# Performance work log

Measured on AMD Instinct MI355X. Metric: run time of the kernel, lower is better.

## Reference

```python
import jax, jax.numpy as jnp
import numpy as np

B, H, W, C = 16, 64, 64, 512
WS, SS, NH = 8, 4, 16
HD = C // NH
N = WS * WS          # tokens per window = 64
NWH, NWW = H // WS, W // WS
NW = NWH * NWW       # windows per image = 64
HID = 2048
EPS = 1e-5

def _rel_pos_index():
    coords = np.stack(np.meshgrid(np.arange(WS), np.arange(WS), indexing='ij'))  # [2,ws,ws]
    cf = coords.reshape(2, -1)                      # [2,N]
    rel = cf[:, :, None] - cf[:, None, :]           # [2,N,N]
    rel = rel.transpose(1, 2, 0).astype(np.int64)   # [N,N,2]
    rel[:, :, 0] += WS - 1
    rel[:, :, 1] += WS - 1
    rel[:, :, 0] *= 2 * WS - 1
    return rel.sum(-1)                              # [N,N]

def _attn_mask():
    img = np.zeros((H, W), dtype=np.float32)
    cnt = 0
    sls = (slice(0, -WS), slice(-WS, -SS), slice(-SS, None))
    for hs in sls:
        for ws_ in sls:
            img[hs, ws_] = cnt
            cnt += 1
    mw = img.reshape(NWH, WS, NWW, WS).transpose(0, 2, 1, 3).reshape(-1, N)  # [nW,N]
    am = mw[:, None, :] - mw[:, :, None]            # [nW,N,N] (unsqueeze(1)-unsqueeze(2))
    return np.where(am != 0, np.float32(-100.0), np.float32(0.0))

_RPI = jnp.asarray(_rel_pos_index())
_AMASK = jnp.asarray(_attn_mask())

def _ln(x, g, b):
    m = jnp.mean(x, -1, keepdims=True)
    v = jnp.mean((x - m) ** 2, -1, keepdims=True)
    return (x - m) * jax.lax.rsqrt(v + EPS) * g + b

def setup_inputs() -> dict:
    key = jax.random.key(0)
    ks = jax.random.split(key, 8)
    s = 0.02
    return {
        'x': jax.random.normal(ks[0], (B, H * W, C), jnp.float32),
        'g1': jnp.ones((C,), jnp.float32), 'b1': jnp.zeros((C,), jnp.float32),
        'qkv_w': jax.random.normal(ks[1], (C, 3 * C), jnp.float32) * s,
        'qkv_b': jnp.zeros((3 * C,), jnp.float32),
        'proj_w': jax.random.normal(ks[2], (C, C), jnp.float32) * s,
        'proj_b': jnp.zeros((C,), jnp.float32),
        'rpb': jax.random.normal(ks[3], ((2 * WS - 1) ** 2, NH), jnp.float32) * s,
        'g2': jnp.ones((C,), jnp.float32), 'b2': jnp.zeros((C,), jnp.float32),
        'fc1_w': jax.random.normal(ks[4], (C, HID), jnp.float32) * s,
        'fc1_b': jnp.zeros((HID,), jnp.float32),
        'fc2_w': jax.random.normal(ks[5], (HID, C), jnp.float32) * s,
        'fc2_b': jnp.zeros((C,), jnp.float32),
    }

def reference(x, g1, b1, qkv_w, qkv_b, proj_w, proj_b, rpb, g2, b2, fc1_w, fc1_b, fc2_w, fc2_b):
    shortcut = x                                    # [B,L,C]
    xn = _ln(x, g1, b1).reshape(B, H, W, C)
    xs = jnp.roll(xn, (-SS, -SS), axis=(1, 2))      # cyclic shift
    # window partition -> [B*nW, N, C]
    xw = xs.reshape(B, NWH, WS, NWW, WS, C).transpose(0, 1, 3, 2, 4, 5).reshape(-1, N, C)
    # attention
    qkv = xw @ qkv_w + qkv_b                        # [Bw,N,3C]
    qkv = qkv.reshape(-1, N, 3, NH, HD).transpose(2, 0, 3, 1, 4)  # [3,Bw,NH,N,HD]
    q, k, v = qkv[0], qkv[1], qkv[2]
    scale = jnp.asarray(HD ** -0.5, xw.dtype)
    attn = jnp.einsum('bhnd,bhmd->bhnm', q, k) * scale            # [Bw,NH,N,N]
    bias = rpb[_RPI.reshape(-1)].reshape(N, N, NH).transpose(2, 0, 1)
    attn = attn + bias[None]
    attn = attn.reshape(B, NW, NH, N, N) + _AMASK[None, :, None]
    attn = jax.nn.softmax(attn.reshape(-1, NH, N, N), axis=-1)
    out = jnp.einsum('bhnm,bhmd->bhnd', attn, v)    # [Bw,NH,N,HD]
    out = out.transpose(0, 2, 1, 3).reshape(-1, N, C)
    out = out @ proj_w + proj_b
    # window reverse -> [B,H,W,C]
    xr = out.reshape(B, NWH, NWW, WS, WS, C).transpose(0, 1, 3, 2, 4, 5).reshape(B, H, W, C)
    xr = jnp.roll(xr, (SS, SS), axis=(1, 2)).reshape(B, H * W, C)
    x = shortcut + xr
    h = _ln(x, g2, b2)
    h = jax.nn.gelu(h @ fc1_w + fc1_b, approximate=False) @ fc2_w + fc2_b
    return x + h
```

## Files before the change

kernel.cpp:

```cpp
#include <hip/hip_runtime.h>
#include <hip/hip_bf16.h>

using f32x4  = __attribute__((ext_vector_type(4))) float;
using bf16x8 = __attribute__((ext_vector_type(8))) short;
using short8 = __attribute__((ext_vector_type(8))) short;
using s16x4  = __attribute__((ext_vector_type(4))) short;

#define DEVINL __device__ __forceinline__

DEVINL short f2bf(float f) {
  unsigned u = __builtin_bit_cast(unsigned, f);
  u += 0x7fffu + ((u >> 16) & 1u);
  return (short)(u >> 16);
}

DEVINL float gelu_fast(float v) {
  float t = __expf(-1.5957691216057308f * (v + 0.044715f * v * v * v));
  return v * __builtin_amdgcn_rcpf(1.0f + t);
}

#define GLDS16(g, l) __builtin_amdgcn_global_load_lds( \
    (const __attribute__((address_space(1))) void*)(g), \
    (__attribute__((address_space(3))) void*)(l), 16, 0, 0)

__global__ __launch_bounds__(256)
void transpose_bf16(const float* __restrict__ in, short* __restrict__ out, int R, int C) {
  int idx = blockIdx.x * 256 + threadIdx.x;
  if (idx >= R * C) return;
  int c = idx / R, r = idx % R;
  out[idx] = f2bf(in[(size_t)r * C + c]);
}

__global__ __launch_bounds__(256)
void bias_expand(const float* __restrict__ rpb, float* __restrict__ BIASF) {
  int idx = blockIdx.x * 256 + threadIdx.x;
  int head = idx >> 12, n = (idx >> 6) & 63, m = idx & 63;
  int i1 = n >> 3, j1 = n & 7, i2 = m >> 3, j2 = m & 7;
  BIASF[idx] = rpb[((i1 - i2 + 7) * 15 + (j1 - j2 + 7)) * 16 + head];
}

template<int REMAP>
__global__ __launch_bounds__(256)
void ln_kernel(const float* __restrict__ X, const float* __restrict__ gamma,
               const float* __restrict__ beta, short* __restrict__ OUT) {
  const int lane = threadIdx.x & 63;
  const int wid  = threadIdx.x >> 6;
  const int t    = blockIdx.x * 4 + wid;
  const float* xp = X + (size_t)t * 512 + lane * 8;
  float4 a = *(const float4*)xp;
  float4 b = *(const float4*)(xp + 4);
  float s = a.x + a.y + a.z + a.w + b.x + b.y + b.z + b.w;
  float q = a.x*a.x + a.y*a.y + a.z*a.z + a.w*a.w
          + b.x*b.x + b.y*b.y + b.z*b.z + b.w*b.w;
#pragma unroll
  for (int d = 1; d < 64; d <<= 1) { s += __shfl_xor(s, d); q += __shfl_xor(q, d); }
  float mean = s * (1.0f / 512.0f);
  float var  = q * (1.0f / 512.0f) - mean * mean;
  float rstd = rsqrtf(var + 1e-5f);
  float4 g0 = *(const float4*)(gamma + lane * 8);
  float4 g1 = *(const float4*)(gamma + lane * 8 + 4);
  float4 b0 = *(const float4*)(beta + lane * 8);
  float4 b1 = *(const float4*)(beta + lane * 8 + 4);
  short8 o;
  o[0] = f2bf((a.x - mean) * rstd * g0.x + b0.x);
  o[1] = f2bf((a.y - mean) * rstd * g0.y + b0.y);
  o[2] = f2bf((a.z - mean) * rstd * g0.z + b0.z);
  o[3] = f2bf((a.w - mean) * rstd * g0.w + b0.w);
  o[4] = f2bf((b.x - mean) * rstd * g1.x + b1.x);
  o[5] = f2bf((b.y - mean) * rstd * g1.y + b1.y);
  o[6] = f2bf((b.z - mean) * rstd * g1.z + b1.z);
  o[7] = f2bf((b.w - mean) * rstd * g1.w + b1.w);
  size_t orow;
  if (REMAP) {
    int bb = t >> 12, l = t & 4095, hh = l >> 6, ww = l & 63;
    int hs = (hh + 60) & 63, ws2 = (ww + 60) & 63;
    orow = (size_t)(bb * 64 + (hs >> 3) * 8 + (ws2 >> 3)) * 64 + (hs & 7) * 8 + (ws2 & 7);
  } else {
    orow = (size_t)t;
  }
  *(short8*)(OUT + orow * 512 + lane * 8) = o;
}

__global__ __launch_bounds__(256)
void attn_core(const short* __restrict__ Q, const short* __restrict__ Kb,
               const short* __restrict__ VT, const float* __restrict__ BIASF,
               short* __restrict__ AOUT) {
  __shared__ short P[4][4096];
  const int tid = threadIdx.x, lane = tid & 63, wid = tid >> 6;
  const int lr = lane & 15, lg = lane >> 4;
  const int gw = blockIdx.x * 4 + wid;
  const int win = gw >> 4, head = gw & 15;
  const int wimg = win & 63, wh = wimg >> 3, ww = wimg & 7;
  const size_t qbase = (size_t)win * 64 * 512 + head * 32;
  short* Pb = P[wid];

  bf16x8 aq[4], bk[4];
#pragma unroll
  for (int tm = 0; tm < 4; ++tm) aq[tm] = *(const bf16x8*)(Q  + qbase + (size_t)(tm * 16 + lr) * 512 + lg * 8);
#pragma unroll
  for (int tn = 0; tn < 4; ++tn) bk[tn] = *(const bf16x8*)(Kb + qbase + (size_t)(tn * 16 + lr) * 512 + lg * 8);
  f32x4 sa[4][4] = {};
#pragma unroll
  for (int tm = 0; tm < 4; ++tm)
#pragma unroll
    for (int tn = 0; tn < 4; ++tn)
      sa[tm][tn] = __builtin_amdgcn_mfma_f32_16x16x32_bf16(aq[tm], bk[tn], sa[tm][tn], 0, 0, 0);

  const float* bias_h = BIASF + head * 4096;
  float inv[4][4];
#pragma unroll
  for (int tm = 0; tm < 4; ++tm) {
#pragma unroll
    for (int e = 0; e < 4; ++e) {
      const int n = tm * 16 + lg * 4 + e;
      const int i1 = n >> 3, j1 = n & 7;
      const int rh1 = (wh == 7) ? 1 + (i1 >> 2) : 0;
      const int rw1 = (ww == 7) ? 1 + (j1 >> 2) : 0;
      float v[4];
      float mx = -3.0e38f;
#pragma unroll
      for (int tn = 0; tn < 4; ++tn) {
        const int m = tn * 16 + lr;
        const int mi = (m >> 3), mj = m & 7;
        const int rh2 = (wh == 7) ? 1 + (mi >> 2) : 0;
        const int rw2 = (ww == 7) ? 1 + (mj >> 2) : 0;
        float val = sa[tm][tn][e] + bias_h[n * 64 + m]
                  + ((rh1 != rh2 || rw1 != rw2) ? -100.0f : 0.0f);
        v[tn] = val;
        mx = fmaxf(mx, val);
      }
#pragma unroll
      for (int d = 1; d < 16; d <<= 1) mx = fmaxf(mx, __shfl_xor(mx, d));
      float sum = 0.f;
#pragma unroll
      for (int tn = 0; tn < 4; ++tn) { v[tn] = __expf(v[tn] - mx); sum += v[tn]; }
#pragma unroll
      for (int d = 1; d < 16; d <<= 1) sum += __shfl_xor(sum, d);
      inv[tm][e] = 1.0f / sum;
      const int sw = (n & 7) << 3;
#pragma unroll
      for (int tn = 0; tn < 4; ++tn) Pb[n * 64 + ((tn * 16 + lr) ^ sw)] = f2bf(v[tn]);
    }
  }
  __syncthreads();

  f32x4 oa[4][2] = {};
  const short* vt = VT + (size_t)win * 32768 + head * 2048;
#pragma unroll
  for (int ks = 0; ks < 2; ++ks) {
    bf16x8 pa[4], bv[2];
#pragma unroll
    for (int tm = 0; tm < 4; ++tm) {
      const int r = tm * 16 + lr;
      pa[tm] = *(const bf16x8*)(Pb + r * 64 + ((ks * 32 + lg * 8) ^ ((r & 7) << 3)));
    }
#pragma unroll
    for (int t2 = 0; t2 < 2; ++t2) bv[t2] = *(const bf16x8*)(vt + (t2 * 16 + lr) * 64 + ks * 32 + lg * 8);
#pragma unroll
    for (int tm = 0; tm < 4; ++tm)
#pragma unroll
      for (int t2 = 0; t2 < 2; ++t2)
        oa[tm][t2] = __builtin_amdgcn_mfma_f32_16x16x32_bf16(pa[tm], bv[t2], oa[tm][t2], 0, 0, 0);
  }
#pragma unroll
  for (int tm = 0; tm < 4; ++tm)
#pragma unroll
    for (int t2 = 0; t2 < 2; ++t2)
#pragma unroll
      for (int e = 0; e < 4; ++e) {
        const int n = tm * 16 + lg * 4 + e;
        AOUT[((size_t)win * 64 + n) * 512 + head * 32 + t2 * 16 + lr] = f2bf(oa[tm][t2][e] * inv[tm][e]);
      }
}

template<int EPI, int K, int NX>
__global__ __launch_bounds__(512, 1)
void gemmBK64(const short* __restrict__ Aa, const short* __restrict__ Bb,
              const float* __restrict__ bias, const float* __restrict__ resid,
              float* __restrict__ outf, short* __restrict__ outh) {
  constexpr int NT = K / 64;
  __shared__ short L[24576];
  const int tid = threadIdx.x;
  const int lane = tid & 63, wid = tid >> 6;
  const int lr = lane & 15, lg = lane >> 4;
  const int wm = wid >> 1, wn = wid & 1;

  const int nwg = gridDim.x;
  const int id = blockIdx.x;
  const int id2 = (id & 7) * (nwg >> 3) + (id >> 3);
  const int mt    = (EPI == 1) ? (id2 % NX) : (id2 / NX);
  const int ntile = (EPI == 1) ? (id2 / NX) : (id2 % NX);
  const int m0 = mt * 256, n0 = ntile * 128;

  const int rr = tid >> 3;
  const int ss = ((tid & 7) ^ (rr & 7)) * 8;
  const short* pA = Aa + (size_t)(m0 + rr) * K + ss;
  const short* pB = Bb + (size_t)(n0 + rr) * K + ss;
  char* Ld = (char*)L + tid * 16;

  const int xr = lr & 7;
  const char* rA0 = (char*)L + (wm * 64 + lr) * 128 + ((lg ^ xr) << 4);
  const char* rA1 = (char*)L + (wm * 64 + lr) * 128 + (((4 + lg) ^ xr) << 4);
  const char* rB0 = (char*)L + 32768 + (wn * 64 + lr) * 128 + ((lg ^ xr) << 4);
  const char* rB1 = (char*)L + 32768 + (wn * 64 + lr) * 128 + (((4 + lg) ^ xr) << 4);

  f32x4 acc[4][4] = {};
  for (int kt = 0; kt < NT; ++kt) {
    const int ko = kt * 64;
    GLDS16(pA + ko,                    Ld);
    GLDS16(pA + ko + (size_t)64  * K,  Ld + 8192);
    GLDS16(pA + ko + (size_t)128 * K,  Ld + 16384);
    GLDS16(pA + ko + (size_t)192 * K,  Ld + 24576);
    GLDS16(pB + ko,                    Ld + 32768);
    GLDS16(pB + ko + (size_t)64  * K,  Ld + 40960);
    __syncthreads();
    bf16x8 a[4], b[4];
#pragma unroll
    for (int i = 0; i < 4; ++i) a[i] = *(const bf16x8*)(rA0 + i * 2048);
#pragma unroll
    for (int j = 0; j < 4; ++j) b[j] = *(const bf16x8*)(rB0 + j * 2048);
#pragma unroll
    for (int i = 0; i < 4; ++i)
#pragma unroll
      for (int j = 0; j < 4; ++j)
        acc[i][j] = __builtin_amdgcn_mfma_f32_16x16x32_bf16(a[i], b[j], acc[i][j], 0, 0, 0);
#pragma unroll
    for (int i = 0; i < 4; ++i) a[i] = *(const bf16x8*)(rA1 + i * 2048);
#pragma unroll
    for (int j = 0; j < 4; ++j) b[j] = *(const bf16x8*)(rB1 + j * 2048);
#pragma unroll
    for (int i = 0; i < 4; ++i)
#pragma unroll
      for (int j = 0; j < 4; ++j)
        acc[i][j] = __builtin_amdgcn_mfma_f32_16x16x32_bf16(a[i], b[j], acc[i][j], 0, 0, 0);
    __syncthreads();
  }

  if (EPI == 1) {
#pragma unroll
    for (int i = 0; i < 4; ++i) {
      const int h0 = m0 + wm * 64 + i * 16 + lg * 4;
      const float4 bi = *(const float4*)(bias + h0);
#pragma unroll
      for (int j = 0; j < 4; ++j) {
        const int tok = n0 + wn * 64 + j * 16 + lr;
        s16x4 o;
        o[0] = f2bf(gelu_fast(acc[i][j][0] + bi.x));
        o[1] = f2bf(gelu_fast(acc[i][j][1] + bi.y));
        o[2] = f2bf(gelu_fast(acc[i][j][2] + bi.z));
        o[3] = f2bf(gelu_fast(acc[i][j][3] + bi.w));
        *(s16x4*)(outh + (size_t)tok * 2048 + h0) = o;
      }
    }
  } else if (EPI == 0) {
#pragma unroll
    for (int j = 0; j < 4; ++j) {
      const int col = n0 + wn * 64 + j * 16 + lr;
      const float bc = bias[col];
#pragma unroll
      for (int i = 0; i < 4; ++i)
#pragma unroll
        for (int e = 0; e < 4; ++e) {
          const int row = m0 + wm * 64 + i * 16 + lg * 4 + e;
          float v = acc[i][j][e] + bc;
          const int wv = row >> 6, n = row & 63;
          const int bb = wv >> 6, wi = wv & 63;
          const int hs = (wi >> 3) * 8 + (n >> 3), ws2 = (wi & 7) * 8 + (n & 7);
          const int hh = (hs + 4) & 63, wwp = (ws2 + 4) & 63;
          const size_t orow = (size_t)bb * 4096 + hh * 64 + wwp;
          outf[orow * 512 + col] = resid[orow * 512 + col] + v;
        }
    }
  } else if (EPI == 2) {
#pragma unroll
    for (int j = 0; j < 4; ++j) {
      const int col = n0 + wn * 64 + j * 16 + lr;
      const float bc = bias[col];
#pragma unroll
      for (int i = 0; i < 4; ++i)
#pragma unroll
        for (int e = 0; e < 4; ++e) {
          const int row = m0 + wm * 64 + i * 16 + lg * 4 + e;
          outf[(size_t)row * 512 + col] = acc[i][j][e] + bc + resid[(size_t)row * 512 + col];
        }
    }
  } else {
    const int seg = n0 >> 9;
#pragma unroll
    for (int j = 0; j < 4; ++j) {
      const int col = n0 + wn * 64 + j * 16 + lr;
      const float bc = bias[col];
#pragma unroll
      for (int i = 0; i < 4; ++i) {
        const int row0 = m0 + wm * 64 + i * 16 + lg * 4;
        if (seg == 2) {
          const int cc = col - 1024;
          s16x4 o;
#pragma unroll
          for (int e = 0; e < 4; ++e) o[e] = f2bf(acc[i][j][e] + bc);
          *(s16x4*)(outh + 67108864 +
                    (size_t)((row0 >> 6) * 16 + (cc >> 5)) * 2048 + (cc & 31) * 64 + (row0 & 63)) = o;
        } else {
#pragma unroll
          for (int e = 0; e < 4; ++e) {
            const int row = row0 + e;
            float v = acc[i][j][e] + bc;
            if (seg == 0) outh[(size_t)row * 512 + col] = f2bf(v * 0.17677669529663687f);
            else          outh[33554432 + (size_t)row * 512 + (col - 512)] = f2bf(v);
          }
        }
      }
    }
  }
}

extern "C" void kernel_launch(void* const* d_in, const int* in_sizes, int n_in,
                              void* d_out, int out_size, void* d_ws, size_t ws_size,
                              hipStream_t stream) {
  (void)in_sizes; (void)n_in; (void)out_size; (void)ws_size;
  const float* x      = (const float*)d_in[0];
  const float* g1     = (const float*)d_in[1];
  const float* b1     = (const float*)d_in[2];
  const float* qkv_w  = (const float*)d_in[3];
  const float* qkv_b  = (const float*)d_in[4];
  const float* proj_w = (const float*)d_in[5];
  const float* proj_b = (const float*)d_in[6];
  const float* rpb    = (const float*)d_in[7];
  const float* g2     = (const float*)d_in[8];
  const float* b2     = (const float*)d_in[9];
  const float* fc1_w  = (const float*)d_in[10];
  const float* fc1_b  = (const float*)d_in[11];
  const float* fc2_w  = (const float*)d_in[12];
  const float* fc2_b  = (const float*)d_in[13];
  float* out = (float*)d_out;
  char* ws = (char*)d_ws;

  short* WQKVT  = (short*)(ws);
  short* WPROJT = (short*)(ws + 1572864);
  short* WFC1T  = (short*)(ws + 2097152);
  short* WFC2T  = (short*)(ws + 4194304);
  float* X2     = (float*)(ws + 6291456);
  float* BIASF  = (float*)(ws + 6291456);
  short* ATT    = (short*)(ws + 140509184);
  short* XW     = (short*)(ws + 207618048);
  short* QB     = (short*)(ws + 274726912);
  short* H1     = XW;
  short* X2N    = ATT;

  transpose_bf16<<<3072, 256, 0, stream>>>(qkv_w,  WQKVT, 512, 1536);
  transpose_bf16<<<1024, 256, 0, stream>>>(proj_w, WPROJT, 512, 512);
  transpose_bf16<<<4096, 256, 0, stream>>>(fc1_w,  WFC1T, 512, 2048);
  transpose_bf16<<<4096, 256, 0, stream>>>(fc2_w,  WFC2T, 2048, 512);
  bias_expand<<<256, 256, 0, stream>>>(rpb, BIASF);

  ln_kernel<1><<<16384, 256, 0, stream>>>(x, g1, b1, XW);
  gemmBK64<3, 512, 12><<<3072, 512, 0, stream>>>(XW, WQKVT, qkv_b, nullptr, nullptr, QB);
  attn_core<<<4096, 256, 0, stream>>>(QB, QB + 33554432, QB + 67108864, BIASF, ATT);
  gemmBK64<0, 512, 4><<<1024, 512, 0, stream>>>(ATT, WPROJT, proj_b, x, X2, nullptr);
  ln_kernel<0><<<16384, 256, 0, stream>>>(X2, g2, b2, X2N);
  gemmBK64<1, 512, 8><<<4096, 512, 0, stream>>>(WFC1T, X2N, fc1_b, nullptr, nullptr, H1);
  gemmBK64<2, 2048, 4><<<1024, 512, 0, stream>>>(H1, WFC2T, fc2_b, X2, out, nullptr);
}
```

Baseline: 843.1 us.

## Store residual stream in bf16 and transpose QKV GEMM operand order

The proj GEMM now writes the post-attention residual X2 as bf16 instead of fp32. A new bf16-input LayerNorm kernel reads it, and the fc2 epilogue reads the bf16 residual back. Separately, the QKV GEMM swaps A/B so weights are the M dimension, and its epilogue is rewritten with vector bias loads and per-element strided V-transpose stores. This cuts memory traffic for the intermediate residual, at the cost of reduced precision in the residual path and a different store pattern for Q/K/V.

Result: no change. 857.7 us (+1.7%).

```diff
diff --git a/kernel.cpp b/kernel.cpp
--- a/kernel.cpp
+++ b/kernel.cpp
@@ -12,6 +12,9 @@
   unsigned u = __builtin_bit_cast(unsigned, f);
   u += 0x7fffu + ((u >> 16) & 1u);
   return (short)(u >> 16);
+}
+DEVINL float bf2f(short h) {
+  return __builtin_bit_cast(float, (unsigned)((unsigned short)h) << 16);
 }
 
 DEVINL float gelu_fast(float v) {
@@ -82,6 +85,40 @@
 }
 
 __global__ __launch_bounds__(256)
+void ln_bf16(const short* __restrict__ X, const float* __restrict__ gamma,
+             const float* __restrict__ beta, short* __restrict__ OUT) {
+  const int lane = threadIdx.x & 63;
+  const int wid  = threadIdx.x >> 6;
+  const int t    = blockIdx.x * 4 + wid;
+  short8 v = *(const short8*)(X + (size_t)t * 512 + lane * 8);
+  float f[8];
+#pragma unroll
+  for (int k = 0; k < 8; ++k) f[k] = bf2f(v[k]);
+  float s = 0.f, q = 0.f;
+#pragma unroll
+  for (int k = 0; k < 8; ++k) { s += f[k]; q += f[k] * f[k]; }
+#pragma unroll
+  for (int d = 1; d < 64; d <<= 1) { s += __shfl_xor(s, d); q += __shfl_xor(q, d); }
+  float mean = s * (1.0f / 512.0f);
+  float var  = q * (1.0f / 512.0f) - mean * mean;
+  float rstd = rsqrtf(var + 1e-5f);
+  float4 g0 = *(const float4*)(gamma + lane * 8);
+  float4 g1 = *(const float4*)(gamma + lane * 8 + 4);
+  float4 b0 = *(const float4*)(beta + lane * 8);
+  float4 b1 = *(const float4*)(beta + lane * 8 + 4);
+  short8 o;
+  o[0] = f2bf((f[0] - mean) * rstd * g0.x + b0.x);
+  o[1] = f2bf((f[1] - mean) * rstd * g0.y + b0.y);
+  o[2] = f2bf((f[2] - mean) * rstd * g0.z + b0.z);
+  o[3] = f2bf((f[3] - mean) * rstd * g0.w + b0.w);
+  o[4] = f2bf((f[4] - mean) * rstd * g1.x + b1.x);
+  o[5] = f2bf((f[5] - mean) * rstd * g1.y + b1.y);
+  o[6] = f2bf((f[6] - mean) * rstd * g1.z + b1.z);
+  o[7] = f2bf((f[7] - mean) * rstd * g1.w + b1.w);
+  *(short8*)(OUT + (size_t)t * 512 + lane * 8) = o;
+}
+
+__global__ __launch_bounds__(256)
 void attn_core(const short* __restrict__ Q, const short* __restrict__ Kb,
                const short* __restrict__ VT, const float* __restrict__ BIASF,
                short* __restrict__ AOUT) {
@@ -177,6 +214,7 @@
 __global__ __launch_bounds__(512, 1)
 void gemmBK64(const short* __restrict__ Aa, const short* __restrict__ Bb,
               const float* __restrict__ bias, const float* __restrict__ resid,
+              const short* __restrict__ residh,
               float* __restrict__ outf, short* __restrict__ outh) {
   constexpr int NT = K / 64;
   __shared__ short L[24576];
@@ -188,8 +226,9 @@
   const int nwg = gridDim.x;
   const int id = blockIdx.x;
   const int id2 = (id & 7) * (nwg >> 3) + (id >> 3);
-  const int mt    = (EPI == 1) ? (id2 % NX) : (id2 / NX);
-  const int ntile = (EPI == 1) ? (id2 / NX) : (id2 % NX);
+  const bool swapped = (EPI == 1 || EPI == 3);
+  const int mt    = swapped ? (id2 % NX) : (id2 / NX);
+  const int ntile = swapped ? (id2 / NX) : (id2 % NX);
   const int m0 = mt * 256, n0 = ntile * 128;
 
   const int rr = tid >> 3;
@@ -268,7 +307,7 @@
           const int hs = (wi >> 3) * 8 + (n >> 3), ws2 = (wi & 7) * 8 + (n & 7);
           const int hh = (hs + 4) & 63, wwp = (ws2 + 4) & 63;
           const size_t orow = (size_t)bb * 4096 + hh * 64 + wwp;
-          outf[orow * 512 + col] = resid[orow * 512 + col] + v;
+          outh[orow * 512 + col] = f2bf(resid[orow * 512 + col] + v);
         }
     }
   } else if (EPI == 2) {
@@ -281,33 +320,42 @@
 #pragma unroll
         for (int e = 0; e < 4; ++e) {
           const int row = m0 + wm * 64 + i * 16 + lg * 4 + e;
-          outf[(size_t)row * 512 + col] = acc[i][j][e] + bc + resid[(size_t)row * 512 + col];
+          outf[(size_t)row * 512 + col] = acc[i][j][e] + bc + bf2f(residh[(size_t)row * 512 + col]);
         }
     }
   } else {
-    const int seg = n0 >> 9;
-#pragma unroll
-    for (int j = 0; j < 4; ++j) {
-      const int col = n0 + wn * 64 + j * 16 + lr;
-      const float bc = bias[col];
-#pragma unroll
-      for (int i = 0; i < 4; ++i) {
-        const int row0 = m0 + wm * 64 + i * 16 + lg * 4;
-        if (seg == 2) {
-          const int cc = col - 1024;
+    const int seg = m0 >> 9;
+    const float qs = 0.17677669529663687f;
+#pragma unroll
+    for (int i = 0; i < 4; ++i) {
+      const int oc0 = m0 + wm * 64 + i * 16 + lg * 4;
+      const float4 bi = *(const float4*)(bias + oc0);
+#pragma unroll
+      for (int j = 0; j < 4; ++j) {
+        const int tok = n0 + wn * 64 + j * 16 + lr;
+        if (seg == 0) {
           s16x4 o;
-#pragma unroll
-          for (int e = 0; e < 4; ++e) o[e] = f2bf(acc[i][j][e] + bc);
-          *(s16x4*)(outh + 67108864 +
-                    (size_t)((row0 >> 6) * 16 + (cc >> 5)) * 2048 + (cc & 31) * 64 + (row0 & 63)) = o;
+          o[0] = f2bf((acc[i][j][0] + bi.x) * qs);
+          o[1] = f2bf((acc[i][j][1] + bi.y) * qs);
+          o[2] = f2bf((acc[i][j][2] + bi.z) * qs);
+          o[3] = f2bf((acc[i][j][3] + bi.w) * qs);
+          *(s16x4*)(outh + (size_t)tok * 512 + oc0) = o;
+        } else if (seg == 1) {
+          s16x4 o;
+          o[0] = f2bf(acc[i][j][0] + bi.x);
+          o[1] = f2bf(acc[i][j][1] + bi.y);
+          o[2] = f2bf(acc[i][j][2] + bi.z);
+          o[3] = f2bf(acc[i][j][3] + bi.w);
+          *(s16x4*)(outh + 33554432 + (size_t)tok * 512 + (oc0 - 512)) = o;
         } else {
-#pragma unroll
-          for (int e = 0; e < 4; ++e) {
-            const int row = row0 + e;
-            float v = acc[i][j][e] + bc;
-            if (seg == 0) outh[(size_t)row * 512 + col] = f2bf(v * 0.17677669529663687f);
-            else          outh[33554432 + (size_t)row * 512 + (col - 512)] = f2bf(v);
-          }
+          const int cc0 = oc0 - 1024;
+          short* vbase = outh + 67108864 +
+              (size_t)((tok >> 6) * 16 + (cc0 >> 5)) * 2048 + (tok & 63);
+          const int d0 = cc0 & 31;
+          vbase[(d0 + 0) * 64] = f2bf(acc[i][j][0] + bi.x);
+          vbase[(d0 + 1) * 64] = f2bf(acc[i][j][1] + bi.y);
+          vbase[(d0 + 2) * 64] = f2bf(acc[i][j][2] + bi.z);
+          vbase[(d0 + 3) * 64] = f2bf(acc[i][j][3] + bi.w);
         }
       }
     }
@@ -339,7 +387,7 @@
   short* WPROJT = (short*)(ws + 1572864);
   short* WFC1T  = (short*)(ws + 2097152);
   short* WFC2T  = (short*)(ws + 4194304);
-  float* X2     = (float*)(ws + 6291456);
+  short* X2B    = (short*)(ws + 6291456);
   float* BIASF  = (float*)(ws + 6291456);
   short* ATT    = (short*)(ws + 140509184);
   short* XW     = (short*)(ws + 207618048);
@@ -354,10 +402,10 @@
   bias_expand<<<256, 256, 0, stream>>>(rpb, BIASF);
 
   ln_kernel<1><<<16384, 256, 0, stream>>>(x, g1, b1, XW);
-  gemmBK64<3, 512, 12><<<3072, 512, 0, stream>>>(XW, WQKVT, qkv_b, nullptr, nullptr, QB);
+  gemmBK64<3, 512, 6><<<3072, 512, 0, stream>>>(WQKVT, XW, qkv_b, nullptr, nullptr, nullptr, QB);
   attn_core<<<4096, 256, 0, stream>>>(QB, QB + 33554432, QB + 67108864, BIASF, ATT);
-  gemmBK64<0, 512, 4><<<1024, 512, 0, stream>>>(ATT, WPROJT, proj_b, x, X2, nullptr);
-  ln_kernel<0><<<16384, 256, 0, stream>>>(X2, g2, b2, X2N);
-  gemmBK64<1, 512, 8><<<4096, 512, 0, stream>>>(WFC1T, X2N, fc1_b, nullptr, nullptr, H1);
-  gemmBK64<2, 2048, 4><<<1024, 512, 0, stream>>>(H1, WFC2T, fc2_b, X2, out, nullptr);
-}
+  gemmBK64<0, 512, 4><<<1024, 512, 0, stream>>>(ATT, WPROJT, proj_b, x, nullptr, nullptr, X2B);
+  ln_bf16<<<16384, 256, 0, stream>>>(X2B, g2, b2, X2N);
+  gemmBK64<1, 512, 8><<<4096, 512, 0, stream>>>(WFC1T, X2N, fc1_b, nullptr, nullptr, nullptr, H1);
+  gemmBK64<2, 2048, 4><<<1024, 512, 0, stream>>>(H1, WFC2T, fc2_b, nullptr, X2B, out, nullptr);
+}
```

## Swap QKV GEMM operands to emit vectorized Q/K stores; merge prep kernels

Applied to the files above, without the earlier changes.

The QKV projection GEMM now computes the transposed product (weights as the M operand, tokens as the N operand), so each lane's four accumulator values are consecutive output channels. Q and K can then be written as packed 4-element bf16 stores with a vector bias load, replacing the old scalar strided stores. V, whose layout is transposed, goes from one packed store to four scalar stores. The four weight-transpose launches and the bias-expansion launch are folded into a single prep kernel to cut launch overhead.

Result: no change. 846.1 us (+0.3%).

```diff
diff --git a/kernel.cpp b/kernel.cpp
--- a/kernel.cpp
+++ b/kernel.cpp
@@ -24,19 +24,31 @@
     (__attribute__((address_space(3))) void*)(l), 16, 0, 0)
 
 __global__ __launch_bounds__(256)
-void transpose_bf16(const float* __restrict__ in, short* __restrict__ out, int R, int C) {
-  int idx = blockIdx.x * 256 + threadIdx.x;
-  if (idx >= R * C) return;
-  int c = idx / R, r = idx % R;
-  out[idx] = f2bf(in[(size_t)r * C + c]);
-}
-
-__global__ __launch_bounds__(256)
-void bias_expand(const float* __restrict__ rpb, float* __restrict__ BIASF) {
-  int idx = blockIdx.x * 256 + threadIdx.x;
-  int head = idx >> 12, n = (idx >> 6) & 63, m = idx & 63;
-  int i1 = n >> 3, j1 = n & 7, i2 = m >> 3, j2 = m & 7;
-  BIASF[idx] = rpb[((i1 - i2 + 7) * 15 + (j1 - j2 + 7)) * 16 + head];
+void prep(const float* __restrict__ qkv_w, const float* __restrict__ proj_w,
+          const float* __restrict__ fc1_w, const float* __restrict__ fc2_w,
+          const float* __restrict__ rpb,
+          short* __restrict__ WQKVT, short* __restrict__ WPROJT,
+          short* __restrict__ WFC1T, short* __restrict__ WFC2T,
+          float* __restrict__ BIASF) {
+  const int b = blockIdx.x, t = threadIdx.x;
+  if (b < 3072) {
+    int idx = b * 256 + t; int c = idx / 512, r = idx % 512;
+    WQKVT[idx] = f2bf(qkv_w[(size_t)r * 1536 + c]);
+  } else if (b < 4096) {
+    int idx = (b - 3072) * 256 + t; int c = idx / 512, r = idx % 512;
+    WPROJT[idx] = f2bf(proj_w[(size_t)r * 512 + c]);
+  } else if (b < 8192) {
+    int idx = (b - 4096) * 256 + t; int c = idx / 512, r = idx % 512;
+    WFC1T[idx] = f2bf(fc1_w[(size_t)r * 2048 + c]);
+  } else if (b < 12288) {
+    int idx = (b - 8192) * 256 + t; int c = idx / 2048, r = idx % 2048;
+    WFC2T[idx] = f2bf(fc2_w[(size_t)r * 512 + c]);
+  } else {
+    int idx = (b - 12288) * 256 + t;
+    int head = idx >> 12, n = (idx >> 6) & 63, m = idx & 63;
+    int i1 = n >> 3, j1 = n & 7, i2 = m >> 3, j2 = m & 7;
+    BIASF[idx] = rpb[((i1 - i2 + 7) * 15 + (j1 - j2 + 7)) * 16 + head];
+  }
 }
 
 template<int REMAP>
@@ -188,8 +200,9 @@
   const int nwg = gridDim.x;
   const int id = blockIdx.x;
   const int id2 = (id & 7) * (nwg >> 3) + (id >> 3);
-  const int mt    = (EPI == 1) ? (id2 % NX) : (id2 / NX);
-  const int ntile = (EPI == 1) ? (id2 / NX) : (id2 % NX);
+  const bool swapped = (EPI == 1 || EPI == 3);
+  const int mt    = swapped ? (id2 % NX) : (id2 / NX);
+  const int ntile = swapped ? (id2 / NX) : (id2 % NX);
   const int m0 = mt * 256, n0 = ntile * 128;
 
   const int rr = tid >> 3;
@@ -285,29 +298,38 @@
         }
     }
   } else {
-    const int seg = n0 >> 9;
-#pragma unroll
-    for (int j = 0; j < 4; ++j) {
-      const int col = n0 + wn * 64 + j * 16 + lr;
-      const float bc = bias[col];
-#pragma unroll
-      for (int i = 0; i < 4; ++i) {
-        const int row0 = m0 + wm * 64 + i * 16 + lg * 4;
-        if (seg == 2) {
-          const int cc = col - 1024;
+    const int seg = m0 >> 9;
+    const float qs = 0.17677669529663687f;
+#pragma unroll
+    for (int i = 0; i < 4; ++i) {
+      const int oc0 = m0 + wm * 64 + i * 16 + lg * 4;
+      const float4 bi = *(const float4*)(bias + oc0);
+#pragma unroll
+      for (int j = 0; j < 4; ++j) {
+        const int tok = n0 + wn * 64 + j * 16 + lr;
+        if (seg == 0) {
           s16x4 o;
-#pragma unroll
-          for (int e = 0; e < 4; ++e) o[e] = f2bf(acc[i][j][e] + bc);
-          *(s16x4*)(outh + 67108864 +
-                    (size_t)((row0 >> 6) * 16 + (cc >> 5)) * 2048 + (cc & 31) * 64 + (row0 & 63)) = o;
+          o[0] = f2bf((acc[i][j][0] + bi.x) * qs);
+          o[1] = f2bf((acc[i][j][1] + bi.y) * qs);
+          o[2] = f2bf((acc[i][j][2] + bi.z) * qs);
+          o[3] = f2bf((acc[i][j][3] + bi.w) * qs);
+          *(s16x4*)(outh + (size_t)tok * 512 + oc0) = o;
+        } else if (seg == 1) {
+          s16x4 o;
+          o[0] = f2bf(acc[i][j][0] + bi.x);
+          o[1] = f2bf(acc[i][j][1] + bi.y);
+          o[2] = f2bf(acc[i][j][2] + bi.z);
+          o[3] = f2bf(acc[i][j][3] + bi.w);
+          *(s16x4*)(outh + 33554432 + (size_t)tok * 512 + (oc0 - 512)) = o;
         } else {
-#pragma unroll
-          for (int e = 0; e < 4; ++e) {
-            const int row = row0 + e;
-            float v = acc[i][j][e] + bc;
-            if (seg == 0) outh[(size_t)row * 512 + col] = f2bf(v * 0.17677669529663687f);
-            else          outh[33554432 + (size_t)row * 512 + (col - 512)] = f2bf(v);
-          }
+          const int cc0 = oc0 - 1024;
+          short* vbase = outh + 67108864 +
+              (size_t)((tok >> 6) * 16 + (cc0 >> 5)) * 2048 + (tok & 63);
+          const int d0 = cc0 & 31;
+          vbase[(d0 + 0) * 64] = f2bf(acc[i][j][0] + bi.x);
+          vbase[(d0 + 1) * 64] = f2bf(acc[i][j][1] + bi.y);
+          vbase[(d0 + 2) * 64] = f2bf(acc[i][j][2] + bi.z);
+          vbase[(d0 + 3) * 64] = f2bf(acc[i][j][3] + bi.w);
         }
       }
     }
@@ -347,14 +369,11 @@
   short* H1     = XW;
   short* X2N    = ATT;
 
-  transpose_bf16<<<3072, 256, 0, stream>>>(qkv_w,  WQKVT, 512, 1536);
-  transpose_bf16<<<1024, 256, 0, stream>>>(proj_w, WPROJT, 512, 512);
-  transpose_bf16<<<4096, 256, 0, stream>>>(fc1_w,  WFC1T, 512, 2048);
-  transpose_bf16<<<4096, 256, 0, stream>>>(fc2_w,  WFC2T, 2048, 512);
-  bias_expand<<<256, 256, 0, stream>>>(rpb, BIASF);
+  prep<<<12544, 256, 0, stream>>>(qkv_w, proj_w, fc1_w, fc2_w, rpb,
+                                  WQKVT, WPROJT, WFC1T, WFC2T, BIASF);
 
   ln_kernel<1><<<16384, 256, 0, stream>>>(x, g1, b1, XW);
-  gemmBK64<3, 512, 12><<<3072, 512, 0, stream>>>(XW, WQKVT, qkv_b, nullptr, nullptr, QB);
+  gemmBK64<3, 512, 6><<<3072, 512, 0, stream>>>(WQKVT, XW, qkv_b, nullptr, nullptr, QB);
   attn_core<<<4096, 256, 0, stream>>>(QB, QB + 33554432, QB + 67108864, BIASF, ATT);
   gemmBK64<0, 512, 4><<<1024, 512, 0, stream>>>(ATT, WPROJT, proj_b, x, X2, nullptr);
   ln_kernel<0><<<16384, 256, 0, stream>>>(X2, g2, b2, X2N);
```
